# Kernel tuning notes

Measured on AMD Instinct MI355X. Metric: run time of the kernel, lower is better.

The kernel has to match this reference:

```python
import jax, jax.numpy as jnp
import numpy as np

N = 100000   # nodes
E = 1600000  # directed edges
D = 128      # feature dim (input = hidden = embedding)
LN_EPS = 1e-5


def setup_inputs() -> dict:
    key = jax.random.key(0)
    ks = jax.random.split(key, 8)
    scale = 1.0 / np.sqrt(D)
    x = jax.random.normal(ks[0], (N, D), dtype=jnp.float32)
    edge_index = jax.random.randint(ks[1], (2, E), 0, N, dtype=jnp.int64)
    W0 = jax.random.normal(ks[2], (D, D), dtype=jnp.float32) * scale
    W1 = jax.random.normal(ks[3], (D, D), dtype=jnp.float32) * scale
    W2 = jax.random.normal(ks[4], (D, D), dtype=jnp.float32) * scale
    b0 = jnp.zeros((D,), jnp.float32)
    b1 = jnp.zeros((D,), jnp.float32)
    b2 = jnp.zeros((D,), jnp.float32)
    ln_g = jnp.ones((D,), jnp.float32)
    ln_b = jnp.zeros((D,), jnp.float32)
    fn_g = jnp.ones((D,), jnp.float32)
    fn_b = jnp.zeros((D,), jnp.float32)
    return {"x": x, "edge_index": edge_index, "W0": W0, "b0": b0,
            "W1": W1, "b1": b1, "W2": W2, "b2": b2,
            "ln_g": ln_g, "ln_b": ln_b, "fn_g": fn_g, "fn_b": fn_b}


def _gcn_conv(x, W, b, src, dst, n):
    # PyG GCNConv: x' = D^{-1/2} (A + I) D^{-1/2} (x W) + b
    h = x @ W                                   # [N, D]
    # add self-loops
    loops = jnp.arange(n, dtype=src.dtype)
    s = jnp.concatenate([src, loops])           # source nodes
    d = jnp.concatenate([dst, loops])           # target nodes
    deg = jax.ops.segment_sum(jnp.ones_like(d, dtype=h.dtype), d, num_segments=n)
    dinv = jnp.where(deg > 0, jax.lax.rsqrt(deg), 0.0)
    norm = dinv[s] * dinv[d]                    # [E+N]
    msg = h[s] * norm[:, None]                  # gather + scale
    out = jax.ops.segment_sum(msg, d, num_segments=n)  # scatter-add at targets
    return out + b


def _layer_norm(x, g, b):
    mu = jnp.mean(x, axis=-1, keepdims=True)
    var = jnp.mean(jnp.square(x - mu), axis=-1, keepdims=True)
    return (x - mu) * jax.lax.rsqrt(var + LN_EPS) * g + b


def reference(x, edge_index, W0, b0, W1, b1, W2, b2, ln_g, ln_b, fn_g, fn_b):
    src, dst = edge_index[0], edge_index[1]
    n = x.shape[0]
    h = jax.nn.relu(_gcn_conv(x, W0, b0, src, dst, n))
    # single middle block (num_gnn_layers=3 -> loop runs for i=1 only)
    identity = h
    h = _layer_norm(h, ln_g, ln_b)
    h = jax.nn.relu(_gcn_conv(h, W1, b1, src, dst, n)) + identity
    h = _gcn_conv(h, W2, b2, src, dst, n)
    return _layer_norm(h, fn_g, fn_b)
```

## Files before the change

### kernel.cpp

```cpp
#include <hip/hip_runtime.h>
#include <hip/hip_bf16.h>

#define DIM 128
#define SB 256
#define NA 256
#define EAMAX 6272
#define BCAP 4096

typedef __attribute__((ext_vector_type(8))) short bf16x8;
typedef __attribute__((ext_vector_type(4))) float f32x4;

__device__ inline float bf2f(unsigned short u) {
    unsigned v = (unsigned)u << 16;
    union { unsigned u; float f; } c; c.u = v; return c.f;
}
__device__ inline unsigned short f2bf(float f) {
    union { __hip_bfloat16 h; unsigned short u; } c;
    c.h = __float2bfloat16(f);
    return c.u;
}
__device__ inline unsigned pk2(float a, float b) {
    return (unsigned)f2bf(a) | ((unsigned)f2bf(b) << 16);
}


__global__ __launch_bounds__(256) void k_hist(const int* __restrict__ dst,
                                              int* __restrict__ histG,
                                              int* __restrict__ bsum,
                                              int E, int EA, int nbuk) {
    __shared__ int h[1024];
    int t = threadIdx.x, blk = blockIdx.x;
    for (int i = t; i < 1024; i += 256) h[i] = 0;
    __syncthreads();
    int lo = blk * EA, hi = min(E, lo + EA);
    for (int i = lo + t; i < hi; i += 256) atomicAdd(&h[dst[i] >> 7], 1);
    __syncthreads();
    for (int bk = t; bk < nbuk; bk += 256) {
        int c = h[bk];
        histG[bk * NA + blk] = c;
        if (c) atomicAdd(&bsum[bk], c);
    }
}

__global__ __launch_bounds__(1024) void k_scan2(int* __restrict__ bsum, int B) {
    __shared__ int s[1024];
    int t = threadIdx.x;
    int v = (t < B) ? bsum[t] : 0;
    s[t] = v;
    __syncthreads();
    for (int off = 1; off < 1024; off <<= 1) {
        int u = (t >= off) ? s[t - off] : 0;
        __syncthreads();
        s[t] += u;
        __syncthreads();
    }
    if (t < B) bsum[t] = s[t] - v;
}

__global__ __launch_bounds__(SB) void k_scan3g(const int* __restrict__ cnt,
                                               const int* __restrict__ bsum,
                                               int* __restrict__ outx, int n) {
    __shared__ int s[SB];
    int t = threadIdx.x;
    int i = blockIdx.x * SB + t;
    int c = (i < n) ? cnt[i] : 0;
    s[t] = c;
    __syncthreads();
    for (int off = 1; off < SB; off <<= 1) {
        int u = (t >= off) ? s[t - off] : 0;
        __syncthreads();
        s[t] += u;
        __syncthreads();
    }
    int excl = bsum[blockIdx.x] + s[t] - c;
    if (i < n) {
        outx[i] = excl;
        if (i == n - 1) outx[n] = excl + c;
    }
}

__global__ __launch_bounds__(256) void k_place(const int* __restrict__ src,
                                               const int* __restrict__ dst,
                                               const int* __restrict__ scannedG,
                                               unsigned* __restrict__ ebuf,
                                               int E, int EA, int nbuk) {
    __shared__ int h[1024];
    __shared__ int dl[1024];
    __shared__ int ws4[4];
    __shared__ unsigned srt[EAMAX];
    __shared__ unsigned short bkt[EAMAX];
    int t = threadIdx.x, blk = blockIdx.x;
    int lo = blk * EA, hi = min(E, lo + EA);

    for (int i = t; i < 1024; i += 256) h[i] = 0;
    __syncthreads();
    for (int i = lo + t; i < hi; i += 256) atomicAdd(&h[dst[i] >> 7], 1);
    __syncthreads();

    {
        int b4 = t * 4;
        int v0 = h[b4], v1 = h[b4 + 1], v2 = h[b4 + 2], v3 = h[b4 + 3];
        int i1 = v0 + v1, i2 = i1 + v2, i3 = i2 + v3;
        int lane = t & 63, wv = t >> 6;
        int sc = i3;
#pragma unroll
        for (int o = 1; o < 64; o <<= 1) {
            int u = __shfl_up(sc, o);
            if (lane >= o) sc += u;
        }
        if (lane == 63) ws4[wv] = sc;
        __syncthreads();
        int woff = 0;
#pragma unroll
        for (int k = 0; k < 4; ++k) woff += (k < wv) ? ws4[k] : 0;
        int tex = woff + sc - i3;
        h[b4] = tex; h[b4 + 1] = tex + v0; h[b4 + 2] = tex + i1; h[b4 + 3] = tex + i2;
    }
    __syncthreads();

    for (int bk = t; bk < nbuk; bk += 256)
        dl[bk] = scannedG[bk * NA + blk] - h[bk];
    __syncthreads();

    for (int i = lo + t; i < hi; i += 256) {
        int d = dst[i];
        int bk = d >> 7;
        unsigned p = ((unsigned)(d & 127) << 17) | (unsigned)src[i];
        int r = atomicAdd(&h[bk], 1);
        srt[r] = p;
        bkt[r] = (unsigned short)bk;
    }
    __syncthreads();

    int m = hi - lo;
    for (int i = t; i < m; i += 256)
        ebuf[dl[bkt[i]] + i] = srt[i];
}

__global__ __launch_bounds__(256) void k_finish(const unsigned* __restrict__ ebuf,
                                                const int* __restrict__ scannedG,
                                                int* __restrict__ offs,
                                                float* __restrict__ dinv,
                                                int* __restrict__ csrc,
                                                int n, int nbuk) {
    __shared__ unsigned eds[BCAP];
    __shared__ unsigned srt[BCAP];
    __shared__ int lcnt[128], lcur[128];
    __shared__ int wsum[2];
    int b = blockIdx.x, t = threadIdx.x;
    int e0 = scannedG[b * NA], e1 = scannedG[(b + 1) * NA];
    int m = min(e1 - e0, BCAP);

    for (int i = t; i < m; i += 256) eds[i] = ebuf[e0 + i];
    if (t < 128) lcnt[t] = 0;
    __syncthreads();
    for (int i = t; i < m; i += 256) atomicAdd(&lcnt[eds[i] >> 17], 1);
    __syncthreads();

    int c = (t < 128) ? lcnt[t] : 0;
    int lane = t & 63, wv = t >> 6;
    int s = c;
#pragma unroll
    for (int o = 1; o < 64; o <<= 1) {
        int u = __shfl_up(s, o);
        if (lane >= o) s += u;
    }
    if (lane == 63 && wv < 2) wsum[wv] = s;
    __syncthreads();
    int excl = s - c + ((wv == 1) ? wsum[0] : 0);
    if (t < 128) {
        int node = b * 128 + t;
        if (node < n) {
            offs[node] = e0 + excl;
            dinv[node] = rsqrtf((float)(c + 1));
        }
        lcur[t] = excl;
    }
    if (b == nbuk - 1 && t == 0) offs[n] = e1;
    __syncthreads();

    for (int i = t; i < m; i += 256) {
        unsigned v = eds[i];
        int r = atomicAdd(&lcur[v >> 17], 1);
        srt[r] = v & 0x1FFFFu;
    }
    __syncthreads();
    for (int i = t; i < m; i += 256) csrc[e0 + i] = (int)srt[i];
}


template <int BF>
__global__ __launch_bounds__(256) void k_gemm(const void* __restrict__ inp,
                                              const float* __restrict__ W,
                                              const float* __restrict__ dinv,
                                              unsigned short* __restrict__ outH, int n) {
    __shared__ unsigned short Wt[DIM * 136];
    int t = threadIdx.x;
#pragma unroll
    for (int i = 0; i < 64; ++i) {
        int idx = i * 256 + t;
        int k = idx >> 7, nn = idx & 127;
        Wt[nn * 136 + k] = f2bf(W[idx]);
    }
    __syncthreads();

    int l = t & 63, w = t >> 6;
    int g = l >> 4, li = l & 15;
    int rbase = blockIdx.x * 128 + w * 32;

    f32x4 acc[2][8];
#pragma unroll
    for (int mt = 0; mt < 2; ++mt)
#pragma unroll
        for (int nt = 0; nt < 8; ++nt) acc[mt][nt] = (f32x4)(0.f);

#pragma unroll
    for (int kk = 0; kk < 4; ++kk) {
        bf16x8 a[2];
#pragma unroll
        for (int mt = 0; mt < 2; ++mt) {
            int row = rbase + mt * 16 + li;
            int rr = (row < n) ? row : (n - 1);
            if (BF) {
                const unsigned short* pb =
                    (const unsigned short*)inp + (size_t)rr * DIM + kk * 32 + g * 8;
                a[mt] = *(const bf16x8*)pb;
            } else {
                const float* p = (const float*)inp + (size_t)rr * DIM + kk * 32 + g * 8;
                float4 v0 = *(const float4*)p;
                float4 v1 = *(const float4*)(p + 4);
                bf16x8 av;
                av[0] = (short)f2bf(v0.x); av[1] = (short)f2bf(v0.y);
                av[2] = (short)f2bf(v0.z); av[3] = (short)f2bf(v0.w);
                av[4] = (short)f2bf(v1.x); av[5] = (short)f2bf(v1.y);
                av[6] = (short)f2bf(v1.z); av[7] = (short)f2bf(v1.w);
                a[mt] = av;
            }
        }
#pragma unroll
        for (int nt = 0; nt < 8; ++nt) {
            bf16x8 bb = *(const bf16x8*)&Wt[(nt * 16 + li) * 136 + kk * 32 + g * 8];
            acc[0][nt] = __builtin_amdgcn_mfma_f32_16x16x32_bf16(a[0], bb, acc[0][nt], 0, 0, 0);
            acc[1][nt] = __builtin_amdgcn_mfma_f32_16x16x32_bf16(a[1], bb, acc[1][nt], 0, 0, 0);
        }
    }

#pragma unroll
    for (int mt = 0; mt < 2; ++mt)
#pragma unroll
        for (int r = 0; r < 4; ++r) {
            int row = rbase + mt * 16 + g * 4 + r;
            if (row < n) {
                float s = dinv[row];
#pragma unroll
                for (int nt = 0; nt < 8; ++nt)
                    outH[(size_t)row * DIM + nt * 16 + li] = f2bf(acc[mt][nt][r] * s);
            }
        }
}


template <int MODE>
__global__ __launch_bounds__(256) void k_agg(const unsigned* __restrict__ H2,
                                             const float* __restrict__ dinv,
                                             const int* __restrict__ offs,
                                             const int* __restrict__ csrc,
                                             const float* __restrict__ bias,
                                             const unsigned* __restrict__ idbf,
                                             unsigned* __restrict__ rawbf,
                                             unsigned* __restrict__ lnbf,
                                             float* __restrict__ outf,
                                             const float* __restrict__ lg,
                                             const float* __restrict__ lb, int n) {
    int wv = threadIdx.x >> 6, lane = threadIdx.x & 63;
    int i = blockIdx.x * 4 + wv;
    if (i >= n) return;

    unsigned u0 = H2[(size_t)i * 64 + lane];
    float ax = bf2f((unsigned short)(u0 & 0xffff));
    float ay = bf2f((unsigned short)(u0 >> 16));

    int s = offs[i], e = offs[i + 1];
    int j = s;
    for (; j + 16 <= e; j += 16) {
        int idx[16];
#pragma unroll
        for (int q = 0; q < 16; ++q) idx[q] = csrc[j + q];
        unsigned uu[16];
#pragma unroll
        for (int q = 0; q < 16; ++q) uu[q] = H2[(size_t)idx[q] * 64 + lane];
#pragma unroll
        for (int q = 0; q < 16; ++q) {
            ax += bf2f((unsigned short)(uu[q] & 0xffff));
            ay += bf2f((unsigned short)(uu[q] >> 16));
        }
    }
    for (; j + 4 <= e; j += 4) {
        unsigned uu[4];
#pragma unroll
        for (int q = 0; q < 4; ++q) uu[q] = H2[(size_t)csrc[j + q] * 64 + lane];
#pragma unroll
        for (int q = 0; q < 4; ++q) {
            ax += bf2f((unsigned short)(uu[q] & 0xffff));
            ay += bf2f((unsigned short)(uu[q] >> 16));
        }
    }
    for (; j < e; ++j) {
        unsigned v = H2[(size_t)csrc[j] * 64 + lane];
        ax += bf2f((unsigned short)(v & 0xffff));
        ay += bf2f((unsigned short)(v >> 16));
    }

    float di = dinv[i];
    float2 bs = ((const float2*)bias)[lane];
    float vx = di * ax + bs.x;
    float vy = di * ay + bs.y;

    float xx, xy;
    if (MODE == 0) { xx = fmaxf(vx, 0.f); xy = fmaxf(vy, 0.f); }
    if (MODE == 1) {
        unsigned idu = idbf[(size_t)i * 64 + lane];
        xx = fmaxf(vx, 0.f) + bf2f((unsigned short)(idu & 0xffff));
        xy = fmaxf(vy, 0.f) + bf2f((unsigned short)(idu >> 16));
    }
    if (MODE == 2) { xx = vx; xy = vy; }

    if (MODE == 0 || MODE == 1)
        rawbf[(size_t)i * 64 + lane] = pk2(xx, xy);

    if (MODE == 0 || MODE == 2) {
        float su = xx + xy;
#pragma unroll
        for (int m = 1; m < 64; m <<= 1) su += __shfl_xor(su, m);
        float mu = su * (1.f / 128.f);
        float dx = xx - mu, dy = xy - mu;
        float q = dx * dx + dy * dy;
#pragma unroll
        for (int m = 1; m < 64; m <<= 1) q += __shfl_xor(q, m);
        float rstd = rsqrtf(q * (1.f / 128.f) + 1e-5f);
        float2 gg = ((const float2*)lg)[lane];
        float2 bb2 = ((const float2*)lb)[lane];
        float ox = dx * rstd * gg.x + bb2.x;
        float oy = dy * rstd * gg.y + bb2.y;
        if (MODE == 0)
            lnbf[(size_t)i * 64 + lane] = pk2(ox, oy);
        else
            ((float2*)(outf + (size_t)i * DIM))[lane] = make_float2(ox, oy);
    }
}


static inline char* alignp(char* p) {
    return (char*)(((size_t)p + 255) & ~(size_t)255);
}

extern "C" void kernel_launch(void* const* d_in, const int* in_sizes, int n_in,
                              void* d_out, int out_size, void* d_ws, size_t ws_size,
                              hipStream_t stream) {
    const float* x   = (const float*)d_in[0];
    const int*   ei  = (const int*)d_in[1];
    const float* W0  = (const float*)d_in[2];
    const float* b0  = (const float*)d_in[3];
    const float* W1  = (const float*)d_in[4];
    const float* b1  = (const float*)d_in[5];
    const float* W2  = (const float*)d_in[6];
    const float* b2  = (const float*)d_in[7];
    const float* lng = (const float*)d_in[8];
    const float* lnb = (const float*)d_in[9];
    const float* fng = (const float*)d_in[10];
    const float* fnb = (const float*)d_in[11];
    float* out = (float*)d_out;

    int n = in_sizes[0] / DIM;
    int E = in_sizes[1] / 2;
    const int* src = ei;
    const int* dst = ei + E;

    int nbuk = (n + 127) >> 7;
    int EA   = (E + NA - 1) / NA;
    int nh   = nbuk * NA;

    char* p = (char*)d_ws;
    unsigned short* H  = (unsigned short*)p; p = alignp(p + (size_t)n * DIM * 2);
    unsigned* hb  = (unsigned*)p;            p = alignp(p + (size_t)n * DIM * 2);
    unsigned* lno = (unsigned*)p;            p = alignp(p + (size_t)n * DIM * 2);
    float* dinv = (float*)p;                 p = alignp(p + (size_t)n * 4);
    int*   offs = (int*)p;                   p = alignp(p + (size_t)(n + 1) * 4);
    int*   csrc = (int*)p;                   p = alignp(p + (size_t)E * 4);
    unsigned* ebuf = (unsigned*)p;           p = alignp(p + (size_t)E * 4);
    int*   histG = (int*)p;                  p = alignp(p + (size_t)nh * 4);
    int*   scannedG = (int*)p;               p = alignp(p + (size_t)(nh + 1) * 4);
    int*   bsum = (int*)p;

    int grid_g = (n + 127) / 128;
    int Bs = (nh + SB - 1) / SB;

    hipMemsetAsync(bsum, 0, (size_t)nbuk * sizeof(int), stream);
    k_hist<<<NA, 256, 0, stream>>>(dst, histG, bsum, E, EA, nbuk);
    k_scan2<<<1, 1024, 0, stream>>>(bsum, nbuk);
    k_scan3g<<<Bs, SB, 0, stream>>>(histG, bsum, scannedG, nh);
    k_place<<<NA, 256, 0, stream>>>(src, dst, scannedG, ebuf, E, EA, nbuk);
    k_finish<<<nbuk, 256, 0, stream>>>(ebuf, scannedG, offs, dinv, csrc, n, nbuk);

    const unsigned* H2 = (const unsigned*)H;
    int grid_a = (n + 3) / 4;

    k_gemm<0><<<grid_g, 256, 0, stream>>>(x, W0, dinv, H, n);
    k_agg<0><<<grid_a, 256, 0, stream>>>(H2, dinv, offs, csrc, b0, nullptr,
                                         hb, lno, nullptr, lng, lnb, n);

    k_gemm<1><<<grid_g, 256, 0, stream>>>(lno, W1, dinv, H, n);
    k_agg<1><<<grid_a, 256, 0, stream>>>(H2, dinv, offs, csrc, b1, hb,
                                         hb, nullptr, nullptr, nullptr, nullptr, n);

    k_gemm<1><<<grid_g, 256, 0, stream>>>(hb, W2, dinv, H, n);
    k_agg<2><<<grid_a, 256, 0, stream>>>(H2, dinv, offs, csrc, b2, nullptr,
                                         nullptr, nullptr, out, fng, fnb, n);
}
```

Baseline: 341.5 us.

## Merge bucket scans into one kernel and reuse histogram in placement

Removes the single-block bucket-sum scan kernel. Each scan block now computes its base offset by reducing all preceding bucket sums directly and scans one bucket's NA per-block counts. The placement kernel reads its per-bucket counts from the global histogram instead of recounting destinations with shared atomics. NA is doubled to 512 and the per-block edge capacity is halved, which changes the grid shape of the histogram and placement kernels. The goal is fewer launches and less redundant work in CSR construction, at the cost of a quadratic prefix reduction over bucket sums.

```diff
diff --git a/kernel.cpp b/kernel.cpp
--- a/kernel.cpp
+++ b/kernel.cpp
@@ -2,9 +2,8 @@
 #include <hip/hip_bf16.h>
 
 #define DIM 128
-#define SB 256
-#define NA 256
-#define EAMAX 6272
+#define NA 512
+#define EAMAX 3136
 #define BCAP 4096
 
 typedef __attribute__((ext_vector_type(8))) short bf16x8;
@@ -42,45 +41,42 @@
     }
 }
 
-__global__ __launch_bounds__(1024) void k_scan2(int* __restrict__ bsum, int B) {
-    __shared__ int s[1024];
-    int t = threadIdx.x;
-    int v = (t < B) ? bsum[t] : 0;
-    s[t] = v;
-    __syncthreads();
-    for (int off = 1; off < 1024; off <<= 1) {
+__global__ __launch_bounds__(NA) void k_scan3g(const int* __restrict__ cnt,
+                                               const int* __restrict__ bsum,
+                                               int* __restrict__ outx, int nbuk) {
+    __shared__ int s[NA];
+    __shared__ int redw[NA / 64];
+    int bk = blockIdx.x, t = threadIdx.x;
+    int lane = t & 63, wv = t >> 6;
+
+    int acc = 0;
+    for (int b = t; b < bk; b += NA) acc += bsum[b];
+#pragma unroll
+    for (int m = 1; m < 64; m <<= 1) acc += __shfl_xor(acc, m);
+    if (lane == 0) redw[wv] = acc;
+    __syncthreads();
+    int base = 0;
+#pragma unroll
+    for (int k = 0; k < NA / 64; ++k) base += redw[k];
+
+    int i = bk * NA + t;
+    int c = cnt[i];
+    s[t] = c;
+    __syncthreads();
+    for (int off = 1; off < NA; off <<= 1) {
         int u = (t >= off) ? s[t - off] : 0;
         __syncthreads();
         s[t] += u;
         __syncthreads();
     }
-    if (t < B) bsum[t] = s[t] - v;
-}
-
-__global__ __launch_bounds__(SB) void k_scan3g(const int* __restrict__ cnt,
-                                               const int* __restrict__ bsum,
-                                               int* __restrict__ outx, int n) {
-    __shared__ int s[SB];
-    int t = threadIdx.x;
-    int i = blockIdx.x * SB + t;
-    int c = (i < n) ? cnt[i] : 0;
-    s[t] = c;
-    __syncthreads();
-    for (int off = 1; off < SB; off <<= 1) {
-        int u = (t >= off) ? s[t - off] : 0;
-        __syncthreads();
-        s[t] += u;
-        __syncthreads();
-    }
-    int excl = bsum[blockIdx.x] + s[t] - c;
-    if (i < n) {
-        outx[i] = excl;
-        if (i == n - 1) outx[n] = excl + c;
-    }
+    int excl = base + s[t] - c;
+    outx[i] = excl;
+    if (bk == nbuk - 1 && t == NA - 1) outx[i + 1] = excl + c;
 }
 
 __global__ __launch_bounds__(256) void k_place(const int* __restrict__ src,
                                                const int* __restrict__ dst,
+                                               const int* __restrict__ histG,
                                                const int* __restrict__ scannedG,
                                                unsigned* __restrict__ ebuf,
                                                int E, int EA, int nbuk) {
@@ -92,9 +88,8 @@
     int t = threadIdx.x, blk = blockIdx.x;
     int lo = blk * EA, hi = min(E, lo + EA);
 
-    for (int i = t; i < 1024; i += 256) h[i] = 0;
-    __syncthreads();
-    for (int i = lo + t; i < hi; i += 256) atomicAdd(&h[dst[i] >> 7], 1);
+    for (int bk = t; bk < 1024; bk += 256)
+        h[bk] = (bk < nbuk) ? histG[bk * NA + blk] : 0;
     __syncthreads();
 
     {
@@ -393,13 +388,11 @@
     int*   bsum = (int*)p;
 
     int grid_g = (n + 127) / 128;
-    int Bs = (nh + SB - 1) / SB;
 
     hipMemsetAsync(bsum, 0, (size_t)nbuk * sizeof(int), stream);
     k_hist<<<NA, 256, 0, stream>>>(dst, histG, bsum, E, EA, nbuk);
-    k_scan2<<<1, 1024, 0, stream>>>(bsum, nbuk);
-    k_scan3g<<<Bs, SB, 0, stream>>>(histG, bsum, scannedG, nh);
-    k_place<<<NA, 256, 0, stream>>>(src, dst, scannedG, ebuf, E, EA, nbuk);
+    k_scan3g<<<nbuk, NA, 0, stream>>>(histG, bsum, scannedG, nbuk);
+    k_place<<<NA, 256, 0, stream>>>(src, dst, histG, scannedG, ebuf, E, EA, nbuk);
     k_finish<<<nbuk, 256, 0, stream>>>(ebuf, scannedG, offs, dinv, csrc, n, nbuk);
 
     const unsigned* H2 = (const unsigned*)H;
```

Result: no change. 345.5 us (+1.2%).
